# Optimization experiments

Measured on AMD Instinct MI355X. Metric: run time of the kernel, lower is better.

The kernel has to match this reference:

```python
import jax, jax.numpy as jnp
import numpy as np

TAU_MEM = 0.02
THRESHOLD = 0.5
RESET_POTENTIAL = 0.0
SURROGATE_BETA = 4.0
LN_EPS = 1e-6

B, T, F_IN, F_OUT = 64, 1024, 512, 512


def fast_sigmoid(x, beta):
    # Continuous fast-sigmoid surrogate spike: 0.5 * (beta*x / (1 + beta*|x|)) + 0.5
    bx = beta * x
    return 0.5 * bx / (1.0 + jnp.abs(bx)) + 0.5


def setup_inputs() -> dict:
    key = jax.random.key(0)
    k1, k2, k3 = jax.random.split(key, 3)
    spikes = jax.random.uniform(k1, (B, T, F_IN), dtype=jnp.float32)
    W = jax.random.normal(k2, (F_IN, F_OUT), dtype=jnp.float32) / np.sqrt(F_IN)
    b = jnp.zeros((F_OUT,), dtype=jnp.float32)
    ln_scale = jnp.ones((F_OUT,), dtype=jnp.float32)
    ln_bias = jnp.zeros((F_OUT,), dtype=jnp.float32)
    return {"spikes": spikes, "W": W, "b": b, "ln_scale": ln_scale, "ln_bias": ln_bias}


def reference(spikes, W, b, ln_scale, ln_bias):
    # Dense projection of input spike trains: [B,T,F_in] -> [B,T,F_out]
    currents = jnp.einsum('bti,io->bto', spikes, W) + b

    alpha = jnp.exp(jnp.float32(-1.0 / TAU_MEM))

    def lif_step(v_mem, cur):
        v_mem = alpha * v_mem + (1.0 - alpha) * cur
        spike = fast_sigmoid(v_mem - THRESHOLD, SURROGATE_BETA)
        v_mem = v_mem * (1.0 - spike) + RESET_POTENTIAL * spike
        return v_mem, spike

    v0 = jnp.zeros((spikes.shape[0], W.shape[1]), dtype=currents.dtype)
    _, out = jax.lax.scan(lif_step, v0, jnp.transpose(currents, (1, 0, 2)))  # [T,B,F]
    out = jnp.transpose(out, (1, 0, 2))  # [B,T,F]

    # LayerNorm over last axis (flax defaults: eps=1e-6, scale & bias)
    mean = jnp.mean(out, axis=-1, keepdims=True)
    var = jnp.var(out, axis=-1, keepdims=True)
    out = (out - mean) * jax.lax.rsqrt(var + LN_EPS) * ln_scale + ln_bias
    return out
```

## Files before the change

kernel.cpp:

```cpp
#include <hip/hip_runtime.h>

#define THREADS 256
#define NBLK 1024

typedef _Float16 half8 __attribute__((ext_vector_type(8)));
typedef float floatx4 __attribute__((ext_vector_type(4)));

__global__ void wcvt_kernel(const float* __restrict__ W, unsigned short* __restrict__ Wt) {
  __shared__ float tile[32][33];
  const int tx = threadIdx.x, ty = threadIdx.y;
  const int nb = blockIdx.x * 32, kb = blockIdx.y * 32;
#pragma unroll
  for (int i = 0; i < 4; ++i)
    tile[ty + 8 * i][tx] = W[(size_t)(kb + ty + 8 * i) * 512 + nb + tx];
  __syncthreads();
#pragma unroll
  for (int i = 0; i < 4; ++i) {
    union { _Float16 h; unsigned short u; } v;
    v.h = (_Float16)tile[tx][ty + 8 * i];
    Wt[(size_t)(nb + ty + 8 * i) * 512 + kb + tx] = v.u;
  }
}

#define ABUF 8192
#define BBASE 16384
#define BBUF 32768

__global__ __launch_bounds__(THREADS, 2) void lif_fused_kernel(
    const float* __restrict__ A, const unsigned short* __restrict__ Wt,
    const float* __restrict__ bias, const float* __restrict__ lnw,
    const float* __restrict__ lnb, float* __restrict__ out) {
  __shared__ uint4 smem4[5120];
  unsigned char* smem = (unsigned char*)smem4;

  const int tid  = threadIdx.x;
  const int lane = tid & 63;
  const int wave = tid >> 6;
  const int wcol = wave;
  const int l15  = lane & 15;
  const int g    = lane >> 4;
  const int rowBase = blockIdx.x * 64;

  const int bslot = (tid & 3) ^ ((tid >> 3) & 3);
  const int aslot = (tid & 7) ^ ((tid >> 3) & 7);
  const unsigned short* bsrc = Wt + (size_t)(tid >> 2) * 512 + bslot * 8;
  const float* asrc = A + (size_t)(rowBase + (tid >> 3)) * 512 + aslot * 4;

  auto stage = [&](int buf, int kk) {
#pragma unroll
    for (int i = 0; i < 8; ++i) {
      int off = BBASE + buf * BBUF + i * 4096 + wave * 1024;
      off = __builtin_amdgcn_readfirstlane(off);
      __builtin_amdgcn_global_load_lds(
          (const __attribute__((address_space(1))) void*)(bsrc + (size_t)i * 32768 + kk * 32),
          (__attribute__((address_space(3))) void*)(smem + off), 16, 0, 0);
    }
#pragma unroll
    for (int j = 0; j < 2; ++j) {
      int off = buf * ABUF + j * 4096 + wave * 1024;
      off = __builtin_amdgcn_readfirstlane(off);
      __builtin_amdgcn_global_load_lds(
          (const __attribute__((address_space(1))) void*)(asrc + (size_t)j * 16384 + kk * 32),
          (__attribute__((address_space(3))) void*)(smem + off), 16, 0, 0);
    }
  };

  const int aswz = l15 & 7;
  const int aOff0 = ((g << 1) ^ aswz) << 4;
  const int aOff1 = aOff0 ^ 16;
  const int aRowOff = l15 * 128;
  const int bRowOff = (wcol * 128 + l15) * 64;
  const int bsw = (g ^ ((l15 >> 1) & 3)) << 4;

  floatx4 acc[4][8];
#pragma unroll
  for (int m = 0; m < 4; ++m)
#pragma unroll
    for (int n = 0; n < 8; ++n)
      acc[m][n] = (floatx4){0.f, 0.f, 0.f, 0.f};

  stage(0, 0);
  stage(1, 1);

#pragma unroll
  for (int k = 0; k < 16; ++k) {
    if (k < 15) {
      asm volatile("s_waitcnt vmcnt(10)" ::: "memory");
    } else {
      asm volatile("s_waitcnt vmcnt(0)" ::: "memory");
    }
    __builtin_amdgcn_s_barrier();
    __builtin_amdgcn_sched_barrier(0);

    const int buf = k & 1;
    const unsigned char* abase = smem + buf * ABUF + aRowOff;
    half8 a[4];
#pragma unroll
    for (int m = 0; m < 4; ++m) {
      float4 lo = *(const float4*)(abase + m * 2048 + aOff0);
      float4 hi = *(const float4*)(abase + m * 2048 + aOff1);
      half8 t;
      t[0] = (_Float16)lo.x; t[1] = (_Float16)lo.y;
      t[2] = (_Float16)lo.z; t[3] = (_Float16)lo.w;
      t[4] = (_Float16)hi.x; t[5] = (_Float16)hi.y;
      t[6] = (_Float16)hi.z; t[7] = (_Float16)hi.w;
      a[m] = t;
    }
    const unsigned char* bbase = smem + BBASE + buf * BBUF + bRowOff + bsw;
    __builtin_amdgcn_s_setprio(1);
#pragma unroll
    for (int n = 0; n < 8; ++n) {
      half8 bf = *(const half8*)(bbase + n * 1024);
      acc[0][n] = __builtin_amdgcn_mfma_f32_16x16x32_f16(a[0], bf, acc[0][n], 0, 0, 0);
      acc[1][n] = __builtin_amdgcn_mfma_f32_16x16x32_f16(a[1], bf, acc[1][n], 0, 0, 0);
      acc[2][n] = __builtin_amdgcn_mfma_f32_16x16x32_f16(a[2], bf, acc[2][n], 0, 0, 0);
      acc[3][n] = __builtin_amdgcn_mfma_f32_16x16x32_f16(a[3], bf, acc[3][n], 0, 0, 0);
    }
    __builtin_amdgcn_s_setprio(0);
    __builtin_amdgcn_sched_barrier(0);
    __builtin_amdgcn_s_barrier();
    __builtin_amdgcn_sched_barrier(0);
    if (k < 14) stage(buf, k + 2);
  }
  __syncthreads();

  float bcol[8], lsc[8], lbc[8];
#pragma unroll
  for (int n = 0; n < 8; ++n) {
    const int col = wcol * 128 + n * 16 + l15;
    bcol[n] = bias[col];
    lsc[n]  = lnw[col];
    lbc[n]  = lnb[col];
  }
#pragma unroll
  for (int m = 0; m < 4; ++m)
#pragma unroll
    for (int n = 0; n < 8; ++n)
#pragma unroll
      for (int r = 0; r < 4; ++r) {
        float x  = acc[m][n][r] + bcol[n] - 0.5f;
        float bx = 4.0f * x;
        acc[m][n][r] = 0.5f * bx / (1.0f + fabsf(bx)) + 0.5f;
      }

  float rs[4][4], rq[4][4];
#pragma unroll
  for (int m = 0; m < 4; ++m)
#pragma unroll
    for (int r = 0; r < 4; ++r) {
      float s = 0.f, q = 0.f;
#pragma unroll
      for (int n = 0; n < 8; ++n) {
        float v = acc[m][n][r];
        s += v;
        q += v * v;
      }
      rs[m][r] = s;
      rq[m][r] = q;
    }
#pragma unroll
  for (int d = 1; d < 16; d <<= 1) {
#pragma unroll
    for (int m = 0; m < 4; ++m)
#pragma unroll
      for (int r = 0; r < 4; ++r) {
        rs[m][r] += __shfl_xor(rs[m][r], d, 16);
        rq[m][r] += __shfl_xor(rq[m][r], d, 16);
      }
  }

  float* redS = (float*)smem4;
  float* redQ = redS + 256;
  float* mv   = redQ + 256;
  if (l15 == 0) {
#pragma unroll
    for (int m = 0; m < 4; ++m)
#pragma unroll
      for (int r = 0; r < 4; ++r) {
        const int row = m * 16 + g * 4 + r;
        redS[row * 4 + wcol] = rs[m][r];
        redQ[row * 4 + wcol] = rq[m][r];
      }
  }
  __syncthreads();
  if (tid < 64) {
    const float S = redS[tid * 4] + redS[tid * 4 + 1] + redS[tid * 4 + 2] + redS[tid * 4 + 3];
    const float Q = redQ[tid * 4] + redQ[tid * 4 + 1] + redQ[tid * 4 + 2] + redQ[tid * 4 + 3];
    const float mean = S * (1.0f / 512.0f);
    const float var  = Q * (1.0f / 512.0f) - mean * mean;
    mv[tid * 2]     = mean;
    mv[tid * 2 + 1] = rsqrtf(var + 1e-6f);
  }
  __syncthreads();

#pragma unroll
  for (int m = 0; m < 4; ++m)
#pragma unroll
    for (int r = 0; r < 4; ++r) {
      const int row  = m * 16 + g * 4 + r;
      const float mean = mv[row * 2];
      const float rstd = mv[row * 2 + 1];
      const size_t base = (size_t)(rowBase + row) * 512;
#pragma unroll
      for (int n = 0; n < 8; ++n) {
        const int col = wcol * 128 + n * 16 + l15;
        out[base + col] = (acc[m][n][r] - mean) * rstd * lsc[n] + lbc[n];
      }
    }
}

extern "C" void kernel_launch(void* const* d_in, const int* in_sizes, int n_in,
                              void* d_out, int out_size, void* d_ws, size_t ws_size,
                              hipStream_t stream) {
  const float* spikes = (const float*)d_in[0];
  const float* W      = (const float*)d_in[1];
  const float* b      = (const float*)d_in[2];
  const float* lnw    = (const float*)d_in[3];
  const float* lnb    = (const float*)d_in[4];
  float* out = (float*)d_out;
  unsigned short* Wt = (unsigned short*)d_ws;

  wcvt_kernel<<<dim3(16, 16), dim3(32, 8), 0, stream>>>(W, Wt);
  lif_fused_kernel<<<NBLK, THREADS, 0, stream>>>(spikes, Wt, b, lnw, lnb, out);
}
```

Baseline: 92.00 us.

## Load A fragments directly to registers and double block rows to 128

The fused GEMM+LIF+LayerNorm kernel now uses 512 threads covering 128 rows per block, so each staged W tile is shared by two row-waves. A is no longer staged through LDS: each wave loads its fp32 A fragments straight into registers one k-chunk ahead. LDS then holds only double-buffered W tiles with 64-wide k chunks. This aims to raise W reuse, cut LDS traffic and barrier count, and remove the A LDS round trip. The costs are higher register pressure from the prefetched A values and a 128 KB LDS footprint, which may limit occupancy.

```diff
diff --git a/kernel.cpp b/kernel.cpp
--- a/kernel.cpp
+++ b/kernel.cpp
@@ -1,7 +1,7 @@
 #include <hip/hip_runtime.h>
 
-#define THREADS 256
-#define NBLK 1024
+#define THREADS 512
+#define NBLK 512
 
 typedef _Float16 half8 __attribute__((ext_vector_type(8)));
 typedef float floatx4 __attribute__((ext_vector_type(4)));
@@ -22,55 +22,45 @@
   }
 }
 
-#define ABUF 8192
-#define BBASE 16384
-#define BBUF 32768
+#define BBUF 65536
 
 __global__ __launch_bounds__(THREADS, 2) void lif_fused_kernel(
     const float* __restrict__ A, const unsigned short* __restrict__ Wt,
     const float* __restrict__ bias, const float* __restrict__ lnw,
     const float* __restrict__ lnb, float* __restrict__ out) {
-  __shared__ uint4 smem4[5120];
+  __shared__ uint4 smem4[8192];
   unsigned char* smem = (unsigned char*)smem4;
 
   const int tid  = threadIdx.x;
   const int lane = tid & 63;
   const int wave = tid >> 6;
-  const int wcol = wave;
+  const int wrow = wave >> 2;
+  const int wcol = wave & 3;
   const int l15  = lane & 15;
   const int g    = lane >> 4;
-  const int rowBase = blockIdx.x * 64;
-
-  const int bslot = (tid & 3) ^ ((tid >> 3) & 3);
-  const int aslot = (tid & 7) ^ ((tid >> 3) & 7);
-  const unsigned short* bsrc = Wt + (size_t)(tid >> 2) * 512 + bslot * 8;
-  const float* asrc = A + (size_t)(rowBase + (tid >> 3)) * 512 + aslot * 4;
-
-  auto stage = [&](int buf, int kk) {
+  const int rowBase = blockIdx.x * 128;
+
+  const int bs = (tid & 7) ^ ((tid >> 3) & 7);
+  const unsigned short* bsrc = Wt + (size_t)(tid >> 3) * 512 + bs * 8;
+
+  auto stageB = [&](int buf, int c) {
 #pragma unroll
     for (int i = 0; i < 8; ++i) {
-      int off = BBASE + buf * BBUF + i * 4096 + wave * 1024;
+      int off = buf * BBUF + i * 8192 + wave * 1024;
       off = __builtin_amdgcn_readfirstlane(off);
       __builtin_amdgcn_global_load_lds(
-          (const __attribute__((address_space(1))) void*)(bsrc + (size_t)i * 32768 + kk * 32),
+          (const __attribute__((address_space(1))) void*)(bsrc + i * 32768 + c * 64),
           (__attribute__((address_space(3))) void*)(smem + off), 16, 0, 0);
     }
-#pragma unroll
-    for (int j = 0; j < 2; ++j) {
-      int off = buf * ABUF + j * 4096 + wave * 1024;
-      off = __builtin_amdgcn_readfirstlane(off);
-      __builtin_amdgcn_global_load_lds(
-          (const __attribute__((address_space(1))) void*)(asrc + (size_t)j * 16384 + kk * 32),
-          (__attribute__((address_space(3))) void*)(smem + off), 16, 0, 0);
-    }
   };
 
-  const int aswz = l15 & 7;
-  const int aOff0 = ((g << 1) ^ aswz) << 4;
-  const int aOff1 = aOff0 ^ 16;
-  const int aRowOff = l15 * 128;
-  const int bRowOff = (wcol * 128 + l15) * 64;
-  const int bsw = (g ^ ((l15 >> 1) & 3)) << 4;
+  const float* ap[4];
+#pragma unroll
+  for (int m = 0; m < 4; ++m)
+    ap[m] = A + (size_t)(rowBase + wrow * 64 + m * 16 + l15) * 512 + g * 8;
+
+  const int bByte0 = (wcol * 128 + l15) * 128 + ((g ^ (l15 & 7)) << 4);
+  const int bByte1 = bByte0 ^ 64;
 
   floatx4 acc[4][8];
 #pragma unroll
@@ -79,48 +69,79 @@
     for (int n = 0; n < 8; ++n)
       acc[m][n] = (floatx4){0.f, 0.f, 0.f, 0.f};
 
-  stage(0, 0);
-  stage(1, 1);
-
-#pragma unroll
-  for (int k = 0; k < 16; ++k) {
-    if (k < 15) {
-      asm volatile("s_waitcnt vmcnt(10)" ::: "memory");
+  float4 ar[4][2][2];
+
+#pragma unroll
+  for (int m = 0; m < 4; ++m)
+#pragma unroll
+    for (int ks = 0; ks < 2; ++ks)
+#pragma unroll
+      for (int h = 0; h < 2; ++h)
+        ar[m][ks][h] = *(const float4*)(ap[m] + ks * 32 + h * 4);
+  stageB(0, 0);
+  stageB(1, 1);
+
+#pragma unroll
+  for (int c = 0; c < 8; ++c) {
+    if (c < 7) {
+      asm volatile("s_waitcnt vmcnt(8)" ::: "memory");
     } else {
       asm volatile("s_waitcnt vmcnt(0)" ::: "memory");
     }
     __builtin_amdgcn_s_barrier();
     __builtin_amdgcn_sched_barrier(0);
 
-    const int buf = k & 1;
-    const unsigned char* abase = smem + buf * ABUF + aRowOff;
-    half8 a[4];
-#pragma unroll
-    for (int m = 0; m < 4; ++m) {
-      float4 lo = *(const float4*)(abase + m * 2048 + aOff0);
-      float4 hi = *(const float4*)(abase + m * 2048 + aOff1);
-      half8 t;
-      t[0] = (_Float16)lo.x; t[1] = (_Float16)lo.y;
-      t[2] = (_Float16)lo.z; t[3] = (_Float16)lo.w;
-      t[4] = (_Float16)hi.x; t[5] = (_Float16)hi.y;
-      t[6] = (_Float16)hi.z; t[7] = (_Float16)hi.w;
-      a[m] = t;
-    }
-    const unsigned char* bbase = smem + BBASE + buf * BBUF + bRowOff + bsw;
-    __builtin_amdgcn_s_setprio(1);
-#pragma unroll
-    for (int n = 0; n < 8; ++n) {
-      half8 bf = *(const half8*)(bbase + n * 1024);
-      acc[0][n] = __builtin_amdgcn_mfma_f32_16x16x32_f16(a[0], bf, acc[0][n], 0, 0, 0);
-      acc[1][n] = __builtin_amdgcn_mfma_f32_16x16x32_f16(a[1], bf, acc[1][n], 0, 0, 0);
-      acc[2][n] = __builtin_amdgcn_mfma_f32_16x16x32_f16(a[2], bf, acc[2][n], 0, 0, 0);
-      acc[3][n] = __builtin_amdgcn_mfma_f32_16x16x32_f16(a[3], bf, acc[3][n], 0, 0, 0);
-    }
-    __builtin_amdgcn_s_setprio(0);
+    const int buf = c & 1;
+    const unsigned char* bb0 = smem + buf * BBUF + bByte0;
+    const unsigned char* bb1 = smem + buf * BBUF + bByte1;
+
+#pragma unroll
+    for (int ks = 0; ks < 2; ++ks) {
+      half8 a0, a1, a2, a3;
+      {
+        half8 t;
+        float4 lo, hi;
+        lo = ar[0][ks][0]; hi = ar[0][ks][1];
+        t[0]=(_Float16)lo.x; t[1]=(_Float16)lo.y; t[2]=(_Float16)lo.z; t[3]=(_Float16)lo.w;
+        t[4]=(_Float16)hi.x; t[5]=(_Float16)hi.y; t[6]=(_Float16)hi.z; t[7]=(_Float16)hi.w;
+        a0 = t;
+        lo = ar[1][ks][0]; hi = ar[1][ks][1];
+        t[0]=(_Float16)lo.x; t[1]=(_Float16)lo.y; t[2]=(_Float16)lo.z; t[3]=(_Float16)lo.w;
+        t[4]=(_Float16)hi.x; t[5]=(_Float16)hi.y; t[6]=(_Float16)hi.z; t[7]=(_Float16)hi.w;
+        a1 = t;
+        lo = ar[2][ks][0]; hi = ar[2][ks][1];
+        t[0]=(_Float16)lo.x; t[1]=(_Float16)lo.y; t[2]=(_Float16)lo.z; t[3]=(_Float16)lo.w;
+        t[4]=(_Float16)hi.x; t[5]=(_Float16)hi.y; t[6]=(_Float16)hi.z; t[7]=(_Float16)hi.w;
+        a2 = t;
+        lo = ar[3][ks][0]; hi = ar[3][ks][1];
+        t[0]=(_Float16)lo.x; t[1]=(_Float16)lo.y; t[2]=(_Float16)lo.z; t[3]=(_Float16)lo.w;
+        t[4]=(_Float16)hi.x; t[5]=(_Float16)hi.y; t[6]=(_Float16)hi.z; t[7]=(_Float16)hi.w;
+        a3 = t;
+      }
+      if (c < 7) {
+#pragma unroll
+        for (int m = 0; m < 4; ++m)
+#pragma unroll
+          for (int h = 0; h < 2; ++h)
+            ar[m][ks][h] = *(const float4*)(ap[m] + (c + 1) * 64 + ks * 32 + h * 4);
+      }
+      const unsigned char* bb = (ks == 0) ? bb0 : bb1;
+      __builtin_amdgcn_s_setprio(1);
+#pragma unroll
+      for (int n = 0; n < 8; ++n) {
+        half8 bf = *(const half8*)(bb + n * 2048);
+        acc[0][n] = __builtin_amdgcn_mfma_f32_16x16x32_f16(a0, bf, acc[0][n], 0, 0, 0);
+        acc[1][n] = __builtin_amdgcn_mfma_f32_16x16x32_f16(a1, bf, acc[1][n], 0, 0, 0);
+        acc[2][n] = __builtin_amdgcn_mfma_f32_16x16x32_f16(a2, bf, acc[2][n], 0, 0, 0);
+        acc[3][n] = __builtin_amdgcn_mfma_f32_16x16x32_f16(a3, bf, acc[3][n], 0, 0, 0);
+      }
+      __builtin_amdgcn_s_setprio(0);
+    }
+
     __builtin_amdgcn_sched_barrier(0);
     __builtin_amdgcn_s_barrier();
     __builtin_amdgcn_sched_barrier(0);
-    if (k < 14) stage(buf, k + 2);
+    if (c < 6) stageB(buf, c + 2);
   }
   __syncthreads();
 
@@ -170,20 +191,20 @@
   }
 
   float* redS = (float*)smem4;
-  float* redQ = redS + 256;
-  float* mv   = redQ + 256;
+  float* redQ = redS + 512;
+  float* mv   = redQ + 512;
   if (l15 == 0) {
 #pragma unroll
     for (int m = 0; m < 4; ++m)
 #pragma unroll
       for (int r = 0; r < 4; ++r) {
-        const int row = m * 16 + g * 4 + r;
+        const int row = wrow * 64 + m * 16 + g * 4 + r;
         redS[row * 4 + wcol] = rs[m][r];
         redQ[row * 4 + wcol] = rq[m][r];
       }
   }
   __syncthreads();
-  if (tid < 64) {
+  if (tid < 128) {
     const float S = redS[tid * 4] + redS[tid * 4 + 1] + redS[tid * 4 + 2] + redS[tid * 4 + 3];
     const float Q = redQ[tid * 4] + redQ[tid * 4 + 1] + redQ[tid * 4 + 2] + redQ[tid * 4 + 3];
     const float mean = S * (1.0f / 512.0f);
@@ -197,7 +218,7 @@
   for (int m = 0; m < 4; ++m)
 #pragma unroll
     for (int r = 0; r < 4; ++r) {
-      const int row  = m * 16 + g * 4 + r;
+      const int row  = wrow * 64 + m * 16 + g * 4 + r;
       const float mean = mv[row * 2];
       const float rstd = mv[row * 2 + 1];
       const size_t base = (size_t)(rowBase + row) * 512;
```

New measurement: 126.1 us. +37.0%, slower.

## Use 8 waves per block with single-buffered 64-wide K stages

Applied to the files above, without the earlier changes.

Doubles the block to 512 threads, splitting the 64-row tile into two wave rows of 32 so each wave holds half the accumulators. The K loop moves from 16 double-buffered 32-wide steps to 8 single-buffered 64-wide stages, each waiting on all loads before computing. The aim is more waves per CU to hide latency and lower register pressure. In exchange, the load of the next stage no longer overlaps the current compute within a block, and overlap must come from other resident waves.

```diff
diff --git a/kernel.cpp b/kernel.cpp
--- a/kernel.cpp
+++ b/kernel.cpp
@@ -1,6 +1,6 @@
 #include <hip/hip_runtime.h>
 
-#define THREADS 256
+#define THREADS 512
 #define NBLK 1024
 
 typedef _Float16 half8 __attribute__((ext_vector_type(8)));
@@ -22,11 +22,9 @@
   }
 }
 
-#define ABUF 8192
 #define BBASE 16384
-#define BBUF 32768
-
-__global__ __launch_bounds__(THREADS, 2) void lif_fused_kernel(
+
+__global__ __launch_bounds__(THREADS, 4) void lif_fused_kernel(
     const float* __restrict__ A, const unsigned short* __restrict__ Wt,
     const float* __restrict__ bias, const float* __restrict__ lnw,
     const float* __restrict__ lnb, float* __restrict__ out) {
@@ -36,92 +34,108 @@
   const int tid  = threadIdx.x;
   const int lane = tid & 63;
   const int wave = tid >> 6;
-  const int wcol = wave;
+  const int wrow = wave >> 2;
+  const int wcol = wave & 3;
   const int l15  = lane & 15;
   const int g    = lane >> 4;
   const int rowBase = blockIdx.x * 64;
 
-  const int bslot = (tid & 3) ^ ((tid >> 3) & 3);
-  const int aslot = (tid & 7) ^ ((tid >> 3) & 7);
-  const unsigned short* bsrc = Wt + (size_t)(tid >> 2) * 512 + bslot * 8;
-  const float* asrc = A + (size_t)(rowBase + (tid >> 3)) * 512 + aslot * 4;
-
-  auto stage = [&](int buf, int kk) {
-#pragma unroll
-    for (int i = 0; i < 8; ++i) {
-      int off = BBASE + buf * BBUF + i * 4096 + wave * 1024;
+  const int arow  = wave * 4 + (lane >> 4);
+  const int aslot = (lane & 15) ^ (arow & 15);
+  const float* asrcA = A + (size_t)(rowBase + arow) * 512 + aslot * 4;
+  const unsigned short* bsrcB =
+      Wt + (size_t)(wave * 8 + (lane >> 3)) * 512 + ((lane & 7) ^ (lane >> 3)) * 8;
+
+  auto stage = [&](int c) {
+#pragma unroll
+    for (int j = 0; j < 2; ++j) {
+      int off = j * 8192 + wave * 1024;
       off = __builtin_amdgcn_readfirstlane(off);
       __builtin_amdgcn_global_load_lds(
-          (const __attribute__((address_space(1))) void*)(bsrc + (size_t)i * 32768 + kk * 32),
+          (const __attribute__((address_space(1))) void*)(asrcA + (size_t)j * 16384 + c * 64),
           (__attribute__((address_space(3))) void*)(smem + off), 16, 0, 0);
     }
 #pragma unroll
-    for (int j = 0; j < 2; ++j) {
-      int off = buf * ABUF + j * 4096 + wave * 1024;
+    for (int i = 0; i < 8; ++i) {
+      int off = BBASE + i * 8192 + wave * 1024;
       off = __builtin_amdgcn_readfirstlane(off);
       __builtin_amdgcn_global_load_lds(
-          (const __attribute__((address_space(1))) void*)(asrc + (size_t)j * 16384 + kk * 32),
+          (const __attribute__((address_space(1))) void*)(bsrcB + (size_t)i * 32768 + c * 64),
           (__attribute__((address_space(3))) void*)(smem + off), 16, 0, 0);
     }
   };
 
-  const int aswz = l15 & 7;
-  const int aOff0 = ((g << 1) ^ aswz) << 4;
-  const int aOff1 = aOff0 ^ 16;
-  const int aRowOff = l15 * 128;
-  const int bRowOff = (wcol * 128 + l15) * 64;
-  const int bsw = (g ^ ((l15 >> 1) & 3)) << 4;
-
-  floatx4 acc[4][8];
-#pragma unroll
-  for (int m = 0; m < 4; ++m)
+  const int aRowB = (wrow * 32 + l15) * 256;
+  const int e0 = (g * 2) ^ l15;
+  const unsigned char* aP00 = smem + aRowB + e0 * 16;
+  const unsigned char* aP01 = smem + aRowB + (e0 ^ 1) * 16;
+  const unsigned char* aP10 = smem + aRowB + (e0 ^ 8) * 16;
+  const unsigned char* aP11 = smem + aRowB + (e0 ^ 9) * 16;
+  const int bRowB = BBASE + (wcol * 128 + l15) * 128;
+  const int f0 = g ^ (l15 & 7);
+  const unsigned char* bP0 = smem + bRowB + f0 * 16;
+  const unsigned char* bP1 = smem + bRowB + (f0 ^ 4) * 16;
+
+  floatx4 acc[2][8];
+#pragma unroll
+  for (int m = 0; m < 2; ++m)
 #pragma unroll
     for (int n = 0; n < 8; ++n)
       acc[m][n] = (floatx4){0.f, 0.f, 0.f, 0.f};
 
-  stage(0, 0);
-  stage(1, 1);
-
-#pragma unroll
-  for (int k = 0; k < 16; ++k) {
-    if (k < 15) {
-      asm volatile("s_waitcnt vmcnt(10)" ::: "memory");
-    } else {
-      asm volatile("s_waitcnt vmcnt(0)" ::: "memory");
-    }
-    __builtin_amdgcn_s_barrier();
-    __builtin_amdgcn_sched_barrier(0);
-
-    const int buf = k & 1;
-    const unsigned char* abase = smem + buf * ABUF + aRowOff;
-    half8 a[4];
-#pragma unroll
-    for (int m = 0; m < 4; ++m) {
-      float4 lo = *(const float4*)(abase + m * 2048 + aOff0);
-      float4 hi = *(const float4*)(abase + m * 2048 + aOff1);
-      half8 t;
-      t[0] = (_Float16)lo.x; t[1] = (_Float16)lo.y;
-      t[2] = (_Float16)lo.z; t[3] = (_Float16)lo.w;
-      t[4] = (_Float16)hi.x; t[5] = (_Float16)hi.y;
-      t[6] = (_Float16)hi.z; t[7] = (_Float16)hi.w;
-      a[m] = t;
-    }
-    const unsigned char* bbase = smem + BBASE + buf * BBUF + bRowOff + bsw;
-    __builtin_amdgcn_s_setprio(1);
-#pragma unroll
-    for (int n = 0; n < 8; ++n) {
-      half8 bf = *(const half8*)(bbase + n * 1024);
-      acc[0][n] = __builtin_amdgcn_mfma_f32_16x16x32_f16(a[0], bf, acc[0][n], 0, 0, 0);
-      acc[1][n] = __builtin_amdgcn_mfma_f32_16x16x32_f16(a[1], bf, acc[1][n], 0, 0, 0);
-      acc[2][n] = __builtin_amdgcn_mfma_f32_16x16x32_f16(a[2], bf, acc[2][n], 0, 0, 0);
-      acc[3][n] = __builtin_amdgcn_mfma_f32_16x16x32_f16(a[3], bf, acc[3][n], 0, 0, 0);
-    }
-    __builtin_amdgcn_s_setprio(0);
+  auto mk = [](float4 lo, float4 hi) {
+    half8 t;
+    t[0] = (_Float16)lo.x; t[1] = (_Float16)lo.y;
+    t[2] = (_Float16)lo.z; t[3] = (_Float16)lo.w;
+    t[4] = (_Float16)hi.x; t[5] = (_Float16)hi.y;
+    t[6] = (_Float16)hi.z; t[7] = (_Float16)hi.w;
+    return t;
+  };
+
+  auto compute = [&]() {
+    {
+      half8 a0 = mk(*(const float4*)aP00, *(const float4*)aP01);
+      half8 a1 = mk(*(const float4*)(aP00 + 4096), *(const float4*)(aP01 + 4096));
+      __builtin_amdgcn_s_setprio(1);
+#pragma unroll
+      for (int n = 0; n < 8; ++n) {
+        half8 bf = *(const half8*)(bP0 + n * 2048);
+        acc[0][n] = __builtin_amdgcn_mfma_f32_16x16x32_f16(a0, bf, acc[0][n], 0, 0, 0);
+        acc[1][n] = __builtin_amdgcn_mfma_f32_16x16x32_f16(a1, bf, acc[1][n], 0, 0, 0);
+      }
+      __builtin_amdgcn_s_setprio(0);
+    }
+    {
+      half8 a0 = mk(*(const float4*)aP10, *(const float4*)aP11);
+      half8 a1 = mk(*(const float4*)(aP10 + 4096), *(const float4*)(aP11 + 4096));
+      __builtin_amdgcn_s_setprio(1);
+#pragma unroll
+      for (int n = 0; n < 8; ++n) {
+        half8 bf = *(const half8*)(bP1 + n * 2048);
+        acc[0][n] = __builtin_amdgcn_mfma_f32_16x16x32_f16(a0, bf, acc[0][n], 0, 0, 0);
+        acc[1][n] = __builtin_amdgcn_mfma_f32_16x16x32_f16(a1, bf, acc[1][n], 0, 0, 0);
+      }
+      __builtin_amdgcn_s_setprio(0);
+    }
+  };
+
+  stage(0);
+  asm volatile("s_waitcnt vmcnt(0)" ::: "memory");
+  __builtin_amdgcn_s_barrier();
+  __builtin_amdgcn_sched_barrier(0);
+
+#pragma unroll 1
+  for (int c = 0; c < 7; ++c) {
+    compute();
     __builtin_amdgcn_sched_barrier(0);
     __builtin_amdgcn_s_barrier();
     __builtin_amdgcn_sched_barrier(0);
-    if (k < 14) stage(buf, k + 2);
-  }
+    stage(c + 1);
+    asm volatile("s_waitcnt vmcnt(0)" ::: "memory");
+    __builtin_amdgcn_s_barrier();
+    __builtin_amdgcn_sched_barrier(0);
+  }
+  compute();
   __syncthreads();
 
   float bcol[8], lsc[8], lbc[8];
@@ -133,7 +147,7 @@
     lbc[n]  = lnb[col];
   }
 #pragma unroll
-  for (int m = 0; m < 4; ++m)
+  for (int m = 0; m < 2; ++m)
 #pragma unroll
     for (int n = 0; n < 8; ++n)
 #pragma unroll
@@ -143,9 +157,9 @@
         acc[m][n][r] = 0.5f * bx / (1.0f + fabsf(bx)) + 0.5f;
       }
 
-  float rs[4][4], rq[4][4];
-#pragma unroll
-  for (int m = 0; m < 4; ++m)
+  float rs[2][4], rq[2][4];
+#pragma unroll
+  for (int m = 0; m < 2; ++m)
 #pragma unroll
     for (int r = 0; r < 4; ++r) {
       float s = 0.f, q = 0.f;
@@ -161,7 +175,7 @@
 #pragma unroll
   for (int d = 1; d < 16; d <<= 1) {
 #pragma unroll
-    for (int m = 0; m < 4; ++m)
+    for (int m = 0; m < 2; ++m)
 #pragma unroll
       for (int r = 0; r < 4; ++r) {
         rs[m][r] += __shfl_xor(rs[m][r], d, 16);
@@ -174,10 +188,10 @@
   float* mv   = redQ + 256;
   if (l15 == 0) {
 #pragma unroll
-    for (int m = 0; m < 4; ++m)
+    for (int m = 0; m < 2; ++m)
 #pragma unroll
       for (int r = 0; r < 4; ++r) {
-        const int row = m * 16 + g * 4 + r;
+        const int row = wrow * 32 + m * 16 + g * 4 + r;
         redS[row * 4 + wcol] = rs[m][r];
         redQ[row * 4 + wcol] = rq[m][r];
       }
@@ -194,10 +208,10 @@
   __syncthreads();
 
 #pragma unroll
-  for (int m = 0; m < 4; ++m)
+  for (int m = 0; m < 2; ++m)
 #pragma unroll
     for (int r = 0; r < 4; ++r) {
-      const int row  = m * 16 + g * 4 + r;
+      const int row  = wrow * 32 + m * 16 + g * 4 + r;
       const float mean = mv[row * 2];
       const float rstd = mv[row * 2 + 1];
       const size_t base = (size_t)(rowBase + row) * 512;
```

Result: no change. 91.48 us (-0.6%).
